# Kernel tuning notes

Measured on AMD Instinct MI355X. Metric: run time of the kernel, lower is better.

Reference implementation:

```python
import jax, jax.numpy as jnp
import numpy as np
from jax import lax

TAU = 2.0      # LIF membrane time constant
VTH = 0.5      # spike threshold
ALPHA = 4.0    # sigmoid surrogate gradient sharpness (spikingjelly default)
EPS = 1e-5     # BatchNorm eps
HEADS = 8

@jax.custom_vjp
def _spike(x):
    return (x >= 0.0).astype(x.dtype)

def _spike_fwd(x):
    return _spike(x), x

def _spike_bwd(x, g):
    s = jax.nn.sigmoid(ALPHA * x)
    return (g * ALPHA * s * (1.0 - s),)

_spike.defvjp(_spike_fwd, _spike_bwd)

def lif(x_seq):
    # multi-step LIF, decay_input=True, hard reset to 0, detach_reset=True
    def step(v, x):
        v = v + (x - v) / TAU
        s = _spike(v - VTH)
        v = v * (1.0 - lax.stop_gradient(s))
        return v, s
    _, s_seq = lax.scan(step, jnp.zeros_like(x_seq[0]), x_seq)
    return s_seq

def bn(x, gamma, beta, mean, var):
    # inference-mode BatchNorm over channel axis 2 of [T,B,C,H,W]
    sh = (1, 1, -1, 1, 1)
    scale = gamma.reshape(sh) / jnp.sqrt(var.reshape(sh) + EPS)
    return (x - mean.reshape(sh)) * scale + beta.reshape(sh)

def conv1x1(x, w, b=None):
    y = jnp.einsum('oc,tbchw->tbohw', w, x)
    if b is not None:
        y = y + b.reshape(1, 1, -1, 1, 1)
    return y

def setup_inputs() -> dict:
    key = jax.random.key(0)
    T, B, C, H, W = 4, 8, 384, 32, 32
    ks = jax.random.split(key, 20)
    s = 1.0 / np.sqrt(C)
    d = {
        'x': jax.random.normal(ks[0], (T, B, C, H, W), jnp.float32),
        'q_w': jax.random.normal(ks[1], (C, C), jnp.float32) * s,
        'k_w': jax.random.normal(ks[2], (C, C), jnp.float32) * s,
        'v_w': jax.random.normal(ks[3], (C, C), jnp.float32) * s,
        'th_w': jax.random.normal(ks[4], (HEADS, HEADS), jnp.float32) * (1.0 / np.sqrt(HEADS)),
        'proj_w': jax.random.normal(ks[5], (C, C), jnp.float32) * s,
        'proj_b': jax.random.normal(ks[6], (C,), jnp.float32) * 0.01,
    }
    for i, p in enumerate(['q', 'k', 'v', 'proj']):
        kk = jax.random.split(ks[7 + i], 4)
        d[f'{p}_gamma'] = 1.0 + 0.1 * jax.random.normal(kk[0], (C,), jnp.float32)
        d[f'{p}_beta'] = 0.1 * jax.random.normal(kk[1], (C,), jnp.float32)
        d[f'{p}_mean'] = 0.1 * jax.random.normal(kk[2], (C,), jnp.float32)
        d[f'{p}_var'] = jax.random.uniform(kk[3], (C,), jnp.float32, 0.5, 1.5)
    return d

def reference(x, q_w, k_w, v_w, th_w, proj_w, proj_b,
              q_gamma, q_beta, q_mean, q_var,
              k_gamma, k_beta, k_mean, k_var,
              v_gamma, v_beta, v_mean, v_var,
              proj_gamma, proj_beta, proj_mean, proj_var):
    T, B, C, H, W = x.shape
    hd = C // HEADS
    N = H * W
    identity = x
    xs = lif(x)  # shortcut_lif

    def branch(w, g, be, m, va):
        return lif(bn(conv1x1(xs, w), g, be, m, va))

    def split_heads(t):  # [T,B,C,H,W] -> [T,B,heads,N,hd]
        return t.reshape(T, B, HEADS, hd, N).transpose(0, 1, 2, 4, 3)

    q = split_heads(branch(q_w, q_gamma, q_beta, q_mean, q_var))
    k = split_heads(branch(k_w, k_gamma, k_beta, k_mean, k_var))
    v = split_heads(branch(v_w, v_gamma, v_beta, v_mean, v_var))

    kv = (k * v).sum(axis=3)                      # [T,B,heads,hd]
    kv = jnp.einsum('oh,tbhd->tbod', th_w, kv)     # talking heads (Conv1d 1x1, no bias)
    kv = lif(kv)[:, :, :, None, :]                 # [T,B,heads,1,hd]

    x_att = q * kv                                 # broadcast over N
    x_att = x_att.transpose(0, 1, 2, 4, 3).reshape(T, B, C, H, W)
    out = bn(conv1x1(x_att, proj_w, proj_b), proj_gamma, proj_beta, proj_mean, proj_var)
    return out + identity
```

## Files before the change

### kernel.cpp

```cpp
#include <hip/hip_runtime.h>
#include <stdint.h>


typedef unsigned short u16;
typedef __attribute__((ext_vector_type(8))) short short8v;
typedef __attribute__((ext_vector_type(4))) float f32x4;

#define AS1 __attribute__((address_space(1)))
#define AS3 __attribute__((address_space(3)))

__device__ __forceinline__ void async16(const void* g, void* l) {
    __builtin_amdgcn_global_load_lds((const AS1 unsigned int*)g,
                                     (AS3 unsigned int*)l, 16, 0, 0);
}
__device__ __forceinline__ f32x4 mfma_bf16(short8v a, short8v b, f32x4 c) {
    return __builtin_amdgcn_mfma_f32_16x16x32_bf16(a, b, c, 0, 0, 0);
}
__device__ __forceinline__ f32x4 mfma_f16(short8v a, short8v b, f32x4 c) {
    return __builtin_amdgcn_mfma_f32_16x16x32_f16(a, b, c, 0, 0, 0);
}

__device__ __forceinline__ u16 f2bf(float f) {
    uint32_t x = __float_as_uint(f);
    return (u16)((x + 0x7FFFu + ((x >> 16) & 1u)) >> 16);
}

#define SPIKE_H ((u16)0x3C00)
#define SPIKE_B ((u16)0x3F80)

__global__ void prep_kernel(const float* __restrict__ qw, const float* __restrict__ kw,
                            const float* __restrict__ vw, const float* __restrict__ pw,
                            u16* __restrict__ Ah, u16* __restrict__ Aproj) {
    int id = blockIdx.x * 256 + threadIdx.x;
    if (id >= 1152 * 384) return;
    int m = id / 384, c = id % 384;
    int br = m / 384, o = m % 384;
    const float* W = (br == 0) ? qw : (br == 1) ? kw : vw;
    float w = W[o * 384 + c];
    union H { _Float16 h; u16 u; } u0, u1;
    u0.h = (_Float16)w;
    float r1 = w - (float)u0.h;
    u1.h = (_Float16)r1;
    u16* row = Ah + (size_t)m * 768;
    row[c] = u0.u;
    row[384 + c] = u1.u;
    if (br == 0) Aproj[o * 384 + c] = f2bf(pw[o * 384 + c]);
}

__global__ __launch_bounds__(256) void lifx_kernel(const float* __restrict__ x,
                                                   u16* __restrict__ xs) {
    __shared__ u16 Tr[64 * 72];
    int b = blockIdx.z, c0 = blockIdx.y * 64, n0 = blockIdx.x * 64;
    int tid = threadIdx.x;
    int nj = (tid & 15) * 4;
    int ci = tid >> 4;
    float v[4][4];
#pragma unroll
    for (int p = 0; p < 4; p++)
#pragma unroll
        for (int e = 0; e < 4; e++) v[p][e] = 0.0f;

    for (int t = 0; t < 4; t++) {
#pragma unroll
        for (int p = 0; p < 4; p++) {
            const float* src = x + ((size_t)((t * 8 + b) * 384 + c0 + p * 16 + ci)) * 1024 + n0 + nj;
            float4 xv = *(const float4*)src;
            float xa[4] = {xv.x, xv.y, xv.z, xv.w};
#pragma unroll
            for (int e = 0; e < 4; e++) {
                float vv = v[p][e];
                vv = __fadd_rn(vv, __fmul_rn(__fsub_rn(xa[e], vv), 0.5f));
                bool sp = (vv >= 0.5f);
                v[p][e] = sp ? 0.0f : vv;
                Tr[(nj + e) * 72 + p * 16 + ci] = sp ? SPIKE_H : (u16)0;
            }
        }
        __syncthreads();
#pragma unroll
        for (int p = 0; p < 4; p++) {
            int nr = p * 16 + (tid >> 4);
            int c4 = (tid & 15) * 4;
            *(ushort4*)(xs + ((size_t)((t * 8 + b) * 1024 + n0 + nr)) * 384 + c0 + c4) =
                *(const ushort4*)&Tr[nr * 72 + c4];
        }
        __syncthreads();
    }
}

__global__ __launch_bounds__(512, 2) void qkv_kernel(
    const u16* __restrict__ Ah, const u16* __restrict__ xs,
    u16* __restrict__ qs, u16* __restrict__ ks, u16* __restrict__ vs,
    const float* __restrict__ qg, const float* __restrict__ qb, const float* __restrict__ qm, const float* __restrict__ qv,
    const float* __restrict__ kg, const float* __restrict__ kb, const float* __restrict__ km, const float* __restrict__ kvr,
    const float* __restrict__ vg, const float* __restrict__ vb, const float* __restrict__ vm, const float* __restrict__ vvr) {
    __shared__ __align__(16) u16 As[3][8192];
    __shared__ __align__(16) u16 Bs[3][16384];
    __shared__ float bnS[128], bnM[128], bnB[128];

    const int b = blockIdx.z, mt = blockIdx.y, nt = blockIdx.x;
    const int m0 = mt * 128, n0 = nt * 64;
    const int branch = mt / 3, o0 = (mt % 3) * 128;
    const int tid = threadIdx.x, wave = tid >> 6, lane = tid & 63;
    const int l15 = lane & 15, quad = lane >> 4;
    const int wmh = wave >> 2;
    const int wn4 = wave & 3;

    const float* g_  = (branch == 0) ? qg : (branch == 1) ? kg : vg;
    const float* be_ = (branch == 0) ? qb : (branch == 1) ? kb : vb;
    const float* m_  = (branch == 0) ? qm : (branch == 1) ? km : vm;
    const float* v_  = (branch == 0) ? qv : (branch == 1) ? kvr : vvr;
    u16* dstp = (branch == 0) ? qs : (branch == 1) ? ks : vs;

    if (tid < 128) {
        int o = o0 + tid;
        bnS[tid] = g_[o] / sqrtf(v_[o] + 1e-5f);
        bnM[tid] = m_[o];
        bnB[tid] = be_[o];
    }

    const int cl = tid >> 3;
    const int cs8 = ((tid & 7) ^ (cl & 7)) * 8;
    const int dst0 = tid * 8;

    const u16* pA0 = Ah + (size_t)(m0 + cl) * 768 + cs8;
    const u16* pA1 = Ah + (size_t)(m0 + 64 + cl) * 768 + cs8;
    const int tB = (cl >> 4) & 3, nB = cl & 15;
    const u16* pB0 = xs + ((size_t)((tB * 8 + b) * 1024 + n0 +  0 + nB)) * 384 + cs8;
    const u16* pB1 = xs + ((size_t)((tB * 8 + b) * 1024 + n0 + 16 + nB)) * 384 + cs8;
    const u16* pB2 = xs + ((size_t)((tB * 8 + b) * 1024 + n0 + 32 + nB)) * 384 + cs8;
    const u16* pB3 = xs + ((size_t)((tB * 8 + b) * 1024 + n0 + 48 + nB)) * 384 + cs8;

    auto stageA = [&](int Tn, int slot) { int kk = Tn * 64;
        async16(pA0 + kk, &As[slot][dst0]);
        async16(pA1 + kk, &As[slot][4096 + dst0]); };
    auto stageB01 = [&](int Tn, int slot) { int kk = Tn * 64;
        int ck = (kk >= 384) ? kk - 384 : kk;
        async16(pB0 + ck, &Bs[slot][dst0]);
        async16(pB1 + ck, &Bs[slot][4096 + dst0]); };
    auto stageB23 = [&](int Tn, int slot) { int kk = Tn * 64;
        int ck = (kk >= 384) ? kk - 384 : kk;
        async16(pB2 + ck, &Bs[slot][8192 + dst0]);
        async16(pB3 + ck, &Bs[slot][12288 + dst0]); };

    const int ch0 = (quad ^ (l15 & 7)) * 8;
    const int ch1 = ((quad + 4) ^ (l15 & 7)) * 8;
    const int arow = (wmh * 64 + l15) * 64;
    const int bcol = (wn4 * 64 + l15) * 64;

    f32x4 acc[4][4];
#pragma unroll
    for (int i = 0; i < 4; i++)
#pragma unroll
        for (int j = 0; j < 4; j++) acc[i][j] = (f32x4){0.f, 0.f, 0.f, 0.f};

    stageA(0, 0); stageB01(0, 0); stageB23(0, 0);
    stageA(1, 1); stageB01(1, 1); stageB23(1, 1);
    asm volatile("s_waitcnt vmcnt(6)\n\ts_barrier" ::: "memory");

    short8v afA[4], bfA[4], afB[4], bfB[4];
    int r = 0, r2 = 2;
#pragma unroll 1
    for (int Tn = 0; Tn < 12; Tn++) {
#pragma unroll
        for (int i = 0; i < 4; i++) afA[i] = *(const short8v*)&As[r][arow + i * 1024 + ch0];
#pragma unroll
        for (int t = 0; t < 4; t++) bfA[t] = *(const short8v*)&Bs[r][bcol + t * 1024 + ch0];
        __builtin_amdgcn_sched_barrier(0);
#pragma unroll
        for (int i = 0; i < 4; i++) afB[i] = *(const short8v*)&As[r][arow + i * 1024 + ch1];
#pragma unroll
        for (int t = 0; t < 4; t++) bfB[t] = *(const short8v*)&Bs[r][bcol + t * 1024 + ch1];
        if (Tn < 10) { stageA(Tn + 2, r2); stageB01(Tn + 2, r2); stageB23(Tn + 2, r2); }
        __builtin_amdgcn_sched_barrier(0);
        __builtin_amdgcn_s_setprio(1);
#pragma unroll
        for (int i = 0; i < 4; i++)
#pragma unroll
            for (int t = 0; t < 4; t++) acc[i][t] = mfma_f16(afA[i], bfA[t], acc[i][t]);
        __builtin_amdgcn_s_setprio(0);
        __builtin_amdgcn_sched_barrier(0);
        __builtin_amdgcn_s_setprio(1);
#pragma unroll
        for (int i = 0; i < 4; i++)
#pragma unroll
            for (int t = 0; t < 4; t++) acc[i][t] = mfma_f16(afB[i], bfB[t], acc[i][t]);
        __builtin_amdgcn_s_setprio(0);
        if (Tn < 10)       asm volatile("s_waitcnt vmcnt(6)\n\ts_barrier" ::: "memory");
        else if (Tn == 10) asm volatile("s_waitcnt vmcnt(0)\n\ts_barrier" ::: "memory");
        r = (r == 2) ? 0 : r + 1;
        r2 = (r2 == 2) ? 0 : r2 + 1;
    }

    const int nn = n0 + wn4 * 16 + l15;
#pragma unroll
    for (int i = 0; i < 4; i++) {
        int co = wmh * 64 + i * 16 + quad * 4;
        float4 s4 = *(const float4*)&bnS[co];
        float4 m4 = *(const float4*)&bnM[co];
        float4 b4 = *(const float4*)&bnB[co];
        float sc[4] = {s4.x, s4.y, s4.z, s4.w};
        float mn[4] = {m4.x, m4.y, m4.z, m4.w};
        float bt[4] = {b4.x, b4.y, b4.z, b4.w};
        u16 sv[4][4];
#pragma unroll
        for (int e = 0; e < 4; e++) {
            float vv = 0.0f;
#pragma unroll
            for (int t = 0; t < 4; t++) {
                float a = acc[i][t][e];
                a = __fadd_rn(__fmul_rn(__fsub_rn(a, mn[e]), sc[e]), bt[e]);
                vv = __fadd_rn(vv, __fmul_rn(__fsub_rn(a, vv), 0.5f));
                bool sp = (vv >= 0.5f);
                vv = sp ? 0.0f : vv;
                sv[t][e] = sp ? SPIKE_B : (u16)0;
            }
        }
#pragma unroll
        for (int t = 0; t < 4; t++) {
            ushort4 o4;
            o4.x = sv[t][0]; o4.y = sv[t][1]; o4.z = sv[t][2]; o4.w = sv[t][3];
            *(ushort4*)(dstp + ((size_t)((t * 8 + b) * 1024 + nn)) * 384 + o0 + co) = o4;
        }
    }
}

__global__ void kvred_kernel(const u16* __restrict__ ks, const u16* __restrict__ vs,
                             float* __restrict__ r) {
    __shared__ float red[384];
    int tb = blockIdx.y, nc = blockIdx.x;
    int tid = threadIdx.x;
    int rr = tid / 48, c8 = tid % 48;
    red[tid] = 0.0f;
    __syncthreads();

    float cnt[8];
#pragma unroll
    for (int e = 0; e < 8; e++) cnt[e] = 0.0f;

    size_t base = ((size_t)(tb * 1024 + nc * 64 + rr)) * 384 + c8 * 8;
#pragma unroll 2
    for (int it = 0; it < 8; it++) {
        size_t off = base + (size_t)it * 8 * 384;
        uint4 ka = *(const uint4*)(ks + off);
        uint4 va = *(const uint4*)(vs + off);
        uint32_t w0 = ka.x & va.x, w1 = ka.y & va.y, w2 = ka.z & va.z, w3 = ka.w & va.w;
        const uint32_t S = SPIKE_B;
        if ((w0 & 0xFFFFu) == S) cnt[0] += 1.0f;
        if ((w0 >> 16) == S)     cnt[1] += 1.0f;
        if ((w1 & 0xFFFFu) == S) cnt[2] += 1.0f;
        if ((w1 >> 16) == S)     cnt[3] += 1.0f;
        if ((w2 & 0xFFFFu) == S) cnt[4] += 1.0f;
        if ((w2 >> 16) == S)     cnt[5] += 1.0f;
        if ((w3 & 0xFFFFu) == S) cnt[6] += 1.0f;
        if ((w3 >> 16) == S)     cnt[7] += 1.0f;
    }
#pragma unroll
    for (int e = 0; e < 8; e++) atomicAdd(&red[c8 * 8 + e], cnt[e]);
    __syncthreads();
    atomicAdd(&r[tb * 384 + tid], red[tid]);
}

__global__ void talking_kernel(const float* __restrict__ r, const float* __restrict__ th,
                               u16* __restrict__ kvs) {
    int id = blockIdx.x * 256 + threadIdx.x;
    if (id >= 8 * 384) return;
    int b = id / 384, c = id % 384;
    int oh = c / 48, d = c % 48;
    float v = 0.0f;
    for (int t = 0; t < 4; t++) {
        const float* rr = r + (t * 8 + b) * 384 + d;
        float s = 0.0f;
#pragma unroll
        for (int h = 0; h < 8; h++) s = __fmaf_rn(th[oh * 8 + h], rr[h * 48], s);
        v = __fadd_rn(v, __fmul_rn(__fsub_rn(s, v), 0.5f));
        bool sp = (v >= 0.5f);
        v = sp ? 0.0f : v;
        kvs[(t * 8 + b) * 384 + c] = sp ? SPIKE_B : (u16)0;
    }
}

__global__ __launch_bounds__(256, 2) void proj_kernel(
    const u16* __restrict__ Aproj, const u16* __restrict__ qs, const u16* __restrict__ kvs,
    const float* __restrict__ xin,
    const float* __restrict__ pb, const float* __restrict__ pg, const float* __restrict__ pbe,
    const float* __restrict__ pm, const float* __restrict__ pv, float* __restrict__ out) {
    __shared__ __align__(16) u16 At[2][8192];
    __shared__ __align__(16) u16 Bt[2][8192];

    int tb = blockIdx.z, mt = blockIdx.y, nt = blockIdx.x;
    int m0 = mt * 128, n0 = nt * 128;
    int tid = threadIdx.x, wave = tid >> 6, lane = tid & 63;
    int l15 = lane & 15, quad = lane >> 4;
    int wm = (wave & 1) * 64, wn = (wave >> 1) * 64;

    const u16* Bsrc = qs + ((size_t)(tb * 1024 + n0)) * 384;
    const u16* mbase = kvs + tb * 384;

    auto stage = [&](int s) {
        int kk = s * 64;
        int buf = s & 1;
#pragma unroll
        for (int ii = 0; ii < 4; ii++) {
            int l = ii * 256 + tid;
            int row = l >> 3;
            int cs = (l & 7) ^ (row & 7);
            async16(Aproj + (size_t)(m0 + row) * 384 + kk + cs * 8, &At[buf][l * 8]);
            async16(Bsrc + (size_t)row * 384 + kk + cs * 8, &Bt[buf][l * 8]);
        }
    };

    f32x4 acc[4][4];
#pragma unroll
    for (int i = 0; i < 4; i++)
#pragma unroll
        for (int j = 0; j < 4; j++) acc[i][j] = (f32x4){0.f, 0.f, 0.f, 0.f};

    stage(0);
    stage(1);

#pragma unroll 1
    for (int kkb = 0; kkb < 6; kkb++) {
        int buf = kkb & 1;
        int kk = kkb * 64;
        if (kkb < 5) asm volatile("s_waitcnt vmcnt(8)\n\ts_barrier" ::: "memory");
        else         asm volatile("s_waitcnt vmcnt(0)\n\ts_barrier" ::: "memory");

#pragma unroll
        for (int h = 0; h < 2; h++) {
            int g = h * 4 + quad;
            short8v msk = *(const short8v*)(mbase + kk + g * 8);
            short8v af[4], bfr[4];
#pragma unroll
            for (int i = 0; i < 4; i++) {
                int row = wm + i * 16 + l15;
                int ch = g ^ (row & 7);
                af[i] = *(const short8v*)&At[buf][row * 64 + ch * 8];
            }
#pragma unroll
            for (int j = 0; j < 4; j++) {
                int nr = wn + j * 16 + l15;
                int ch = g ^ (nr & 7);
                bfr[j] = *(const short8v*)&Bt[buf][nr * 64 + ch * 8] & msk;
            }
            __builtin_amdgcn_s_setprio(1);
#pragma unroll
            for (int i = 0; i < 4; i++)
#pragma unroll
                for (int j = 0; j < 4; j++) acc[i][j] = mfma_bf16(af[i], bfr[j], acc[i][j]);
            __builtin_amdgcn_s_setprio(0);
        }

        asm volatile("s_waitcnt lgkmcnt(0)\n\ts_barrier" ::: "memory");
        if (kkb + 2 < 6) stage(kkb + 2);
    }

#pragma unroll
    for (int i = 0; i < 4; i++) {
#pragma unroll
        for (int e = 0; e < 4; e++) {
            int o = m0 + wm + i * 16 + quad * 4 + e;
            float scale = pg[o] / sqrtf(pv[o] + 1e-5f);
            float mean = pm[o], beta = pbe[o], bias = pb[o];
#pragma unroll
            for (int j = 0; j < 4; j++) {
                int n = n0 + wn + j * 16 + l15;
                size_t idx = ((size_t)tb * 384 + o) * 1024 + n;
                float y = __fadd_rn(acc[i][j][e], bias);
                y = __fadd_rn(__fmul_rn(__fsub_rn(y, mean), scale), beta);
                out[idx] = __fadd_rn(y, xin[idx]);
            }
        }
    }
}

extern "C" void kernel_launch(void* const* d_in, const int* in_sizes, int n_in,
                              void* d_out, int out_size, void* d_ws, size_t ws_size,
                              hipStream_t stream) {
    (void)in_sizes; (void)n_in; (void)out_size; (void)ws_size;
    const float* x  = (const float*)d_in[0];
    const float* qw = (const float*)d_in[1];
    const float* kw = (const float*)d_in[2];
    const float* vw = (const float*)d_in[3];
    const float* th = (const float*)d_in[4];
    const float* pw = (const float*)d_in[5];
    const float* pb = (const float*)d_in[6];
    const float* qg = (const float*)d_in[7],  *qbe = (const float*)d_in[8];
    const float* qm = (const float*)d_in[9],  *qv  = (const float*)d_in[10];
    const float* kg = (const float*)d_in[11], *kbe = (const float*)d_in[12];
    const float* km = (const float*)d_in[13], *kv_ = (const float*)d_in[14];
    const float* vg = (const float*)d_in[15], *vbe = (const float*)d_in[16];
    const float* vm = (const float*)d_in[17], *vv_ = (const float*)d_in[18];
    const float* pg = (const float*)d_in[19], *pbe = (const float*)d_in[20];
    const float* pm = (const float*)d_in[21], *pv  = (const float*)d_in[22];
    float* out = (float*)d_out;

    char* w = (char*)d_ws;
    const size_t SPIKES = (size_t)32 * 1024 * 384 * 2;
    u16* xs    = (u16*)(w);
    u16* qs    = (u16*)(w + SPIKES);
    u16* ks    = (u16*)(w + 2 * SPIKES);
    u16* vs    = (u16*)(w + 3 * SPIKES);
    u16* Ah    = (u16*)(w + 4 * SPIKES);
    u16* Aproj = (u16*)(w + 4 * SPIKES + 1769472);
    float* r   = (float*)(w + 4 * SPIKES + 1769472 + 294912);
    u16* kvs   = (u16*)(w + 4 * SPIKES + 1769472 + 294912 + 49152);

    hipMemsetAsync(r, 0, 32 * 384 * sizeof(float), stream);

    prep_kernel<<<1728, 256, 0, stream>>>(qw, kw, vw, pw, Ah, Aproj);
    lifx_kernel<<<dim3(16, 6, 8), 256, 0, stream>>>(x, xs);
    qkv_kernel<<<dim3(16, 9, 8), 512, 0, stream>>>(Ah, xs, qs, ks, vs,
                                                   qg, qbe, qm, qv,
                                                   kg, kbe, km, kv_,
                                                   vg, vbe, vm, vv_);
    kvred_kernel<<<dim3(16, 32), 384, 0, stream>>>(ks, vs, r);
    talking_kernel<<<12, 256, 0, stream>>>(r, th, kvs);
    proj_kernel<<<dim3(8, 3, 32), 256, 0, stream>>>(Aproj, qs, kvs, x, pb, pg, pbe, pm, pv, out);
}
```

Measured before the change: 264.3 us.

## Drop kv atomics and memset, restage proj pipeline, cache BN params in LDS

The kv reduction now writes per-chunk partial sums to a larger workspace buffer instead of using shared and global atomics. That removes the memset launch, and the talking-heads kernel sums the 16 partials itself. The projection GEMM changes from a two-deep prefetch to issuing the next stage at the top of each iteration, with sched_barriers splitting LDS fragment loads from two MFMA groups. Its epilogue BatchNorm parameters are precomputed once into LDS. The simpler pipeline may hide less global-load latency, and the talking kernel does more reads.

```diff
diff --git a/kernel.cpp b/kernel.cpp
--- a/kernel.cpp
+++ b/kernel.cpp
@@ -225,13 +225,11 @@
 }
 
 __global__ void kvred_kernel(const u16* __restrict__ ks, const u16* __restrict__ vs,
-                             float* __restrict__ r) {
-    __shared__ float red[384];
+                             float* __restrict__ r2) {
+    __shared__ float red[8][384];
     int tb = blockIdx.y, nc = blockIdx.x;
     int tid = threadIdx.x;
     int rr = tid / 48, c8 = tid % 48;
-    red[tid] = 0.0f;
-    __syncthreads();
 
     float cnt[8];
 #pragma unroll
@@ -255,12 +253,15 @@
         if ((w3 >> 16) == S)     cnt[7] += 1.0f;
     }
 #pragma unroll
-    for (int e = 0; e < 8; e++) atomicAdd(&red[c8 * 8 + e], cnt[e]);
+    for (int e = 0; e < 8; e++) red[rr][c8 * 8 + e] = cnt[e];
     __syncthreads();
-    atomicAdd(&r[tb * 384 + tid], red[tid]);
-}
-
-__global__ void talking_kernel(const float* __restrict__ r, const float* __restrict__ th,
+    float s = 0.0f;
+#pragma unroll
+    for (int q = 0; q < 8; q++) s += red[q][tid];
+    r2[((size_t)(tb * 16 + nc)) * 384 + tid] = s;
+}
+
+__global__ void talking_kernel(const float* __restrict__ r2, const float* __restrict__ th,
                                u16* __restrict__ kvs) {
     int id = blockIdx.x * 256 + threadIdx.x;
     if (id >= 8 * 384) return;
@@ -268,10 +269,15 @@
     int oh = c / 48, d = c % 48;
     float v = 0.0f;
     for (int t = 0; t < 4; t++) {
-        const float* rr = r + (t * 8 + b) * 384 + d;
+        const float* rr = r2 + ((size_t)((t * 8 + b) * 16)) * 384 + d;
         float s = 0.0f;
 #pragma unroll
-        for (int h = 0; h < 8; h++) s = __fmaf_rn(th[oh * 8 + h], rr[h * 48], s);
+        for (int h = 0; h < 8; h++) {
+            float kvsum = 0.0f;
+#pragma unroll
+            for (int nc = 0; nc < 16; nc++) kvsum += rr[nc * 384 + h * 48];
+            s = __fmaf_rn(th[oh * 8 + h], kvsum, s);
+        }
         v = __fadd_rn(v, __fmul_rn(__fsub_rn(s, v), 0.5f));
         bool sp = (v >= 0.5f);
         v = sp ? 0.0f : v;
@@ -286,6 +292,7 @@
     const float* __restrict__ pm, const float* __restrict__ pv, float* __restrict__ out) {
     __shared__ __align__(16) u16 At[2][8192];
     __shared__ __align__(16) u16 Bt[2][8192];
+    __shared__ float eS[128], eM[128], eB[128], eBi[128];
 
     int tb = blockIdx.z, mt = blockIdx.y, nt = blockIdx.x;
     int m0 = mt * 128, n0 = nt * 128;
@@ -295,6 +302,14 @@
 
     const u16* Bsrc = qs + ((size_t)(tb * 1024 + n0)) * 384;
     const u16* mbase = kvs + tb * 384;
+
+    if (tid < 128) {
+        int o = m0 + tid;
+        eS[tid] = pg[o] / sqrtf(pv[o] + 1e-5f);
+        eM[tid] = pm[o];
+        eB[tid] = pbe[o];
+        eBi[tid] = pb[o];
+    }
 
     auto stage = [&](int s) {
         int kk = s * 64;
@@ -316,51 +331,54 @@
         for (int j = 0; j < 4; j++) acc[i][j] = (f32x4){0.f, 0.f, 0.f, 0.f};
 
     stage(0);
-    stage(1);
+    __syncthreads();
 
 #pragma unroll 1
     for (int kkb = 0; kkb < 6; kkb++) {
         int buf = kkb & 1;
         int kk = kkb * 64;
-        if (kkb < 5) asm volatile("s_waitcnt vmcnt(8)\n\ts_barrier" ::: "memory");
-        else         asm volatile("s_waitcnt vmcnt(0)\n\ts_barrier" ::: "memory");
-
-#pragma unroll
-        for (int h = 0; h < 2; h++) {
-            int g = h * 4 + quad;
-            short8v msk = *(const short8v*)(mbase + kk + g * 8);
-            short8v af[4], bfr[4];
-#pragma unroll
-            for (int i = 0; i < 4; i++) {
-                int row = wm + i * 16 + l15;
-                int ch = g ^ (row & 7);
-                af[i] = *(const short8v*)&At[buf][row * 64 + ch * 8];
-            }
-#pragma unroll
-            for (int j = 0; j < 4; j++) {
-                int nr = wn + j * 16 + l15;
-                int ch = g ^ (nr & 7);
-                bfr[j] = *(const short8v*)&Bt[buf][nr * 64 + ch * 8] & msk;
-            }
-            __builtin_amdgcn_s_setprio(1);
-#pragma unroll
-            for (int i = 0; i < 4; i++)
-#pragma unroll
-                for (int j = 0; j < 4; j++) acc[i][j] = mfma_bf16(af[i], bfr[j], acc[i][j]);
-            __builtin_amdgcn_s_setprio(0);
-        }
-
-        asm volatile("s_waitcnt lgkmcnt(0)\n\ts_barrier" ::: "memory");
-        if (kkb + 2 < 6) stage(kkb + 2);
+        if (kkb < 5) stage(kkb + 1);
+        __builtin_amdgcn_sched_barrier(0);
+
+        short8v msk0 = *(const short8v*)(mbase + kk + quad * 8);
+        short8v msk1 = *(const short8v*)(mbase + kk + (4 + quad) * 8);
+        short8v afA[4], bfA[4], afB[4], bfB[4];
+#pragma unroll
+        for (int i = 0; i < 4; i++) {
+            int row = wm + i * 16 + l15;
+            afA[i] = *(const short8v*)&At[buf][row * 64 + ((quad) ^ (row & 7)) * 8];
+            afB[i] = *(const short8v*)&At[buf][row * 64 + ((4 + quad) ^ (row & 7)) * 8];
+        }
+#pragma unroll
+        for (int j = 0; j < 4; j++) {
+            int nr = wn + j * 16 + l15;
+            bfA[j] = *(const short8v*)&Bt[buf][nr * 64 + ((quad) ^ (nr & 7)) * 8] & msk0;
+            bfB[j] = *(const short8v*)&Bt[buf][nr * 64 + ((4 + quad) ^ (nr & 7)) * 8] & msk1;
+        }
+        __builtin_amdgcn_sched_barrier(0);
+        __builtin_amdgcn_s_setprio(1);
+#pragma unroll
+        for (int i = 0; i < 4; i++)
+#pragma unroll
+            for (int j = 0; j < 4; j++) acc[i][j] = mfma_bf16(afA[i], bfA[j], acc[i][j]);
+        __builtin_amdgcn_s_setprio(0);
+        __builtin_amdgcn_sched_barrier(0);
+        __builtin_amdgcn_s_setprio(1);
+#pragma unroll
+        for (int i = 0; i < 4; i++)
+#pragma unroll
+            for (int j = 0; j < 4; j++) acc[i][j] = mfma_bf16(afB[i], bfB[j], acc[i][j]);
+        __builtin_amdgcn_s_setprio(0);
+        if (kkb < 5) asm volatile("s_waitcnt vmcnt(0)\n\ts_barrier" ::: "memory");
     }
 
 #pragma unroll
     for (int i = 0; i < 4; i++) {
 #pragma unroll
         for (int e = 0; e < 4; e++) {
-            int o = m0 + wm + i * 16 + quad * 4 + e;
-            float scale = pg[o] / sqrtf(pv[o] + 1e-5f);
-            float mean = pm[o], beta = pbe[o], bias = pb[o];
+            int co = wm + i * 16 + quad * 4 + e;
+            int o = m0 + co;
+            float scale = eS[co], mean = eM[co], beta = eB[co], bias = eBi[co];
 #pragma unroll
             for (int j = 0; j < 4; j++) {
                 int n = n0 + wn + j * 16 + l15;
@@ -402,10 +420,8 @@
     u16* vs    = (u16*)(w + 3 * SPIKES);
     u16* Ah    = (u16*)(w + 4 * SPIKES);
     u16* Aproj = (u16*)(w + 4 * SPIKES + 1769472);
-    float* r   = (float*)(w + 4 * SPIKES + 1769472 + 294912);
-    u16* kvs   = (u16*)(w + 4 * SPIKES + 1769472 + 294912 + 49152);
-
-    hipMemsetAsync(r, 0, 32 * 384 * sizeof(float), stream);
+    float* r2  = (float*)(w + 4 * SPIKES + 1769472 + 294912);
+    u16* kvs   = (u16*)(w + 4 * SPIKES + 1769472 + 294912 + 786432);
 
     prep_kernel<<<1728, 256, 0, stream>>>(qw, kw, vw, pw, Ah, Aproj);
     lifx_kernel<<<dim3(16, 6, 8), 256, 0, stream>>>(x, xs);
@@ -413,7 +429,7 @@
                                                    qg, qbe, qm, qv,
                                                    kg, kbe, km, kv_,
                                                    vg, vbe, vm, vv_);
-    kvred_kernel<<<dim3(16, 32), 384, 0, stream>>>(ks, vs, r);
-    talking_kernel<<<12, 256, 0, stream>>>(r, th, kvs);
+    kvred_kernel<<<dim3(16, 32), 384, 0, stream>>>(ks, vs, r2);
+    talking_kernel<<<12, 256, 0, stream>>>(r2, th, kvs);
     proj_kernel<<<dim3(8, 3, 32), 256, 0, stream>>>(Aproj, qs, kvs, x, pb, pg, pbe, pm, pv, out);
 }
```

After: 367.5 us. 39.0% more time.
